# Performance work log

Measured on AMD Instinct MI355X. Metric: run time of the kernel, lower is better.

## Reference

```python
import jax, jax.numpy as jnp
import numpy as np

N_NODES = 10000
N_EDGES = 640000
IN_FEAT = 128
OUT_FEAT = 256


def setup_inputs() -> dict:
    key = jax.random.key(0)
    k_h, k_src, k_dst, k_w, k_b = jax.random.split(key, 5)
    h = jax.random.normal(k_h, (N_NODES, IN_FEAT), dtype=jnp.float32)
    src = jax.random.randint(k_src, (N_EDGES,), 0, N_NODES, dtype=jnp.int64)
    dst = jax.random.randint(k_dst, (N_EDGES,), 0, N_NODES, dtype=jnp.int64)
    W = jax.random.normal(k_w, (2 * IN_FEAT, OUT_FEAT), dtype=jnp.float32) * 0.05
    b = jax.random.normal(k_b, (OUT_FEAT,), dtype=jnp.float32) * 0.05
    return {"h": h, "src": src, "dst": dst, "W": W, "b": b}


def reference(h, src, dst, W, b):
    # Message passing: copy_u('h') then mean-reduce over incoming edges (by dst).
    msgs = h[src]                                   # [E, in_feat] gather
    summed = jax.ops.segment_sum(msgs, dst, num_segments=N_NODES)   # [N, in_feat]
    deg = jax.ops.segment_sum(jnp.ones((src.shape[0],), h.dtype), dst,
                              num_segments=N_NODES)                 # [N]
    h_N = jnp.where(deg[:, None] > 0, summed / jnp.maximum(deg, 1.0)[:, None], 0.0)
    # Concat self + neighbor mean, then dense linear.
    h_total = jnp.concatenate([h, h_N], axis=1)     # [N, 2*in_feat]
    return h_total @ W + b                          # [N, out_feat]
```

## Files before the change

### kernel.cpp

```cpp
#include <hip/hip_runtime.h>
#include <hip/hip_bf16.h>

#define NN 10000
#define NE 640000
#define SB 250
#define EPB 2560
#define NR 625
#define CW 32
#define CE 31
#define CONVB 512
#define ZROW 16000

typedef __attribute__((ext_vector_type(8))) short bf16x8;
typedef __attribute__((ext_vector_type(4))) float f32x4;

__device__ __forceinline__ unsigned packbf(float x, float y) {
  __hip_bfloat16 a = __float2bfloat16(x);
  __hip_bfloat16 c = __float2bfloat16(y);
  unsigned short ua = __builtin_bit_cast(unsigned short, a);
  unsigned short uc = __builtin_bit_cast(unsigned short, c);
  return (unsigned)ua | ((unsigned)uc << 16);
}
__device__ __forceinline__ float blo(unsigned u) { return __uint_as_float(u << 16); }
__device__ __forceinline__ float bhi(unsigned u) { return __uint_as_float(u & 0xffff0000u); }

__global__ __launch_bounds__(256) void kA_scatter_conv(
    const float* __restrict__ h, const int* __restrict__ src,
    const int* __restrict__ dst, const float* __restrict__ W,
    unsigned* __restrict__ gbuf, unsigned* __restrict__ hb32,
    uint4* __restrict__ wpk) {
  int t = threadIdx.x;
  int blk = blockIdx.x;
  if (blk < SB) {
    __shared__ int lc[NR];
    for (int i = t; i < NR; i += 256) lc[i] = 0;
    __syncthreads();
    int base = blk * EPB;
    unsigned dv[10], sv[10];
#pragma unroll
    for (int i = 0; i < 10; i++) {
      int e = base + t + i * 256;
      dv[i] = (unsigned)dst[e] & 0x3fffu;
      sv[i] = (unsigned)src[e] & 0x3fffu;
    }
#pragma unroll
    for (int i = 0; i < 10; i++) {
      int range = (int)(dv[i] >> 4);
      if (range >= NR) range = NR - 1;
      int r = atomicAdd(&lc[range], 1);
      if (r < CE)
        gbuf[((size_t)range * SB + blk) * CW + 1 + r] = ((dv[i] & 15u) << 14) | sv[i];
    }
    __syncthreads();
    for (int i = t; i < NR; i += 256)
      gbuf[((size_t)i * SB + blk) * CW] = (unsigned)lc[i];
  } else {
    int tid = (blk - SB) * 256 + t;
    const float4* h4 = (const float4*)h;
    for (int j = tid; j < NN * 32; j += CONVB * 256) {
      float4 v = h4[j];
      uint2 p;
      p.x = packbf(v.x, v.y);
      p.y = packbf(v.z, v.w);
      *(uint2*)(hb32 + (size_t)j * 2) = p;
    }
    if (tid < 64) hb32[(size_t)ZROW * 64 + tid] = 0u;
    if (tid < 8192) {
      int tt = tid & 255, bnks = tid >> 8;
      int ks = bnks & 7, bn = bnks >> 3;
      int w = tt >> 6, l = tt & 63, kb = l >> 4, lm = l & 15;
      int col = bn * 64 + w * 16 + lm;
      int k0 = ks * 32 + kb * 8;
      uint4 p;
      p.x = packbf(W[(k0 + 0) * 256 + col], W[(k0 + 1) * 256 + col]);
      p.y = packbf(W[(k0 + 2) * 256 + col], W[(k0 + 3) * 256 + col]);
      p.z = packbf(W[(k0 + 4) * 256 + col], W[(k0 + 5) * 256 + col]);
      p.w = packbf(W[(k0 + 6) * 256 + col], W[(k0 + 7) * 256 + col]);
      wpk[tid] = p;
    }
  }
}

__global__ __launch_bounds__(256) void k2_agg_gemm(
    const unsigned* __restrict__ gbuf, const unsigned* __restrict__ hb32,
    const uint4* __restrict__ wpk, const float* __restrict__ bias,
    float* __restrict__ out) {
  __shared__ __align__(16) unsigned short As[16][264];
  __shared__ __align__(16) unsigned short cbuf[16][128];
  __shared__ int lcnt[16];
  __shared__ int tdeg[16];
  int t = threadIdx.x;
  int bm = blockIdx.x;

  const unsigned* chunk = gbuf + ((size_t)bm * SB + (t < SB ? t : SB - 1)) * CW;
  uint4 c0 = *(const uint4*)chunk;
  uint4 c1 = *(const uint4*)(chunk + 4);

  if (t < 16) lcnt[t] = 0;

  {
    int row = t >> 4, c4 = t & 15;
    uint4 v = *(const uint4*)(hb32 + (size_t)(bm * 16 + row) * 64 + c4 * 4);
    *(uint4*)(&As[row][c4 * 8]) = v;
  }
  __syncthreads();

  if (t < SB) {
    int c = (int)(c0.x & 0x3fu);
    int kk = c < CE ? c : CE;
    auto route = [&](unsigned v) {
      int dstlo = (int)(v >> 14) & 15;
      unsigned s = v & 0x3fffu;
      int pos = atomicAdd(&lcnt[dstlo], 1);
      if (pos < 128) cbuf[dstlo][pos] = (unsigned short)s;
    };
    if (kk > 0) route(c0.y);
    if (kk > 1) route(c0.z);
    if (kk > 2) route(c0.w);
    if (kk > 3) route(c1.x);
    if (kk > 4) route(c1.y);
    if (kk > 5) route(c1.z);
    if (kk > 6) route(c1.w);
    for (int j = 7; j < kk; j++) route(chunk[1 + j]);
  }
  __syncthreads();

  if (t < 16) {
    int d = lcnt[t];
    tdeg[t] = d;
    int n = d < 128 ? d : 128;
    int np = (n + 7) & ~7;
    for (int j = n; j < np; j++) cbuf[t][j] = (unsigned short)ZROW;
    lcnt[t] = np;
  }
  __syncthreads();

  int w = t >> 6, l = t & 63;
  int g = l >> 4, lm = l & 15;
#pragma unroll
  for (int i = 0; i < 4; i++) {
    int row = w * 4 + i;
    int np = lcnt[row];
    int deg = tdeg[row];
    float a0 = 0.f, a1 = 0.f, a2 = 0.f, a3 = 0.f;
    float a4 = 0.f, a5 = 0.f, a6 = 0.f, a7 = 0.f;
    for (int e = 0; e < np; e += 8) {
      int s0 = cbuf[row][e + g];
      int s1 = cbuf[row][e + 4 + g];
      uint4 u0 = *(const uint4*)(hb32 + (size_t)s0 * 64 + lm * 4);
      uint4 u1 = *(const uint4*)(hb32 + (size_t)s1 * 64 + lm * 4);
      a0 += blo(u0.x) + blo(u1.x);
      a1 += bhi(u0.x) + bhi(u1.x);
      a2 += blo(u0.y) + blo(u1.y);
      a3 += bhi(u0.y) + bhi(u1.y);
      a4 += blo(u0.z) + blo(u1.z);
      a5 += bhi(u0.z) + bhi(u1.z);
      a6 += blo(u0.w) + blo(u1.w);
      a7 += bhi(u0.w) + bhi(u1.w);
    }
    a0 += __shfl_xor(a0, 16); a1 += __shfl_xor(a1, 16);
    a2 += __shfl_xor(a2, 16); a3 += __shfl_xor(a3, 16);
    a4 += __shfl_xor(a4, 16); a5 += __shfl_xor(a5, 16);
    a6 += __shfl_xor(a6, 16); a7 += __shfl_xor(a7, 16);
    a0 += __shfl_xor(a0, 32); a1 += __shfl_xor(a1, 32);
    a2 += __shfl_xor(a2, 32); a3 += __shfl_xor(a3, 32);
    a4 += __shfl_xor(a4, 32); a5 += __shfl_xor(a5, 32);
    a6 += __shfl_xor(a6, 32); a7 += __shfl_xor(a7, 32);
    float inv = (deg > 0) ? 1.f / (float)deg : 0.f;
    if (g == 0) {
      uint4 p;
      p.x = packbf(a0 * inv, a1 * inv);
      p.y = packbf(a2 * inv, a3 * inv);
      p.z = packbf(a4 * inv, a5 * inv);
      p.w = packbf(a6 * inv, a7 * inv);
      *(uint4*)(&As[row][128 + lm * 8]) = p;
    }
  }
  __syncthreads();

  int kb = g;
#pragma unroll
  for (int bn = 0; bn < 4; bn++) {
    int col = bn * 64 + w * 16 + lm;
    f32x4 acc = (f32x4){0.f, 0.f, 0.f, 0.f};
#pragma unroll
    for (int ks = 0; ks < 8; ks++) {
      uint4 braw = wpk[(bn * 8 + ks) * 256 + t];
      bf16x8 bfr = __builtin_bit_cast(bf16x8, braw);
      uint4 araw = *(const uint4*)(&As[lm][ks * 32 + kb * 8]);
      bf16x8 af = __builtin_bit_cast(bf16x8, araw);
      acc = __builtin_amdgcn_mfma_f32_16x16x32_bf16(af, bfr, acc, 0, 0, 0);
    }
    float biasf = bias[col];
#pragma unroll
    for (int reg = 0; reg < 4; reg++) {
      int m = bm * 16 + kb * 4 + reg;
      out[(size_t)m * 256 + col] = acc[reg] + biasf;
    }
  }
}

extern "C" void kernel_launch(void* const* d_in, const int* in_sizes, int n_in,
                              void* d_out, int out_size, void* d_ws, size_t ws_size,
                              hipStream_t stream) {
  const float* h = (const float*)d_in[0];
  const int* src = (const int*)d_in[1];
  const int* dst = (const int*)d_in[2];
  const float* W = (const float*)d_in[3];
  const float* b = (const float*)d_in[4];
  float* out = (float*)d_out;

  char* ws = (char*)d_ws;
  unsigned* gbuf = (unsigned*)(ws + 0);
  unsigned* hb32 = (unsigned*)(ws + 20000000);
  uint4* wpk = (uint4*)(ws + 24194304);

  kA_scatter_conv<<<SB + CONVB, 256, 0, stream>>>(h, src, dst, W, gbuf, hb32, wpk);
  k2_agg_gemm<<<NR, 256, 0, stream>>>(gbuf, hb32, wpk, b, out);
}
```

Baseline: 96.18 us.

## Halve scatter blocks, prefetch larger edge chunks, unroll gather loop, hoist bias

The edge scatter now uses half as many blocks, each binning twice as many edges. Each (range, block) chunk therefore holds about twice as many entries, and the aggregation kernel has half as many chunks to read. The aggregation kernel prefetches the first 16 words of each chunk into registers, unrolls the neighbour gather to 16 edges per iteration for more loads in flight, and loads the bias before the MFMA loop. The workspace offsets shrink to match the smaller bucket buffer. The risks are more register pressure and a higher chance of a chunk overflowing its 31-entry capacity, although that stays unlikely.

```diff
diff --git a/kernel.cpp b/kernel.cpp
--- a/kernel.cpp
+++ b/kernel.cpp
@@ -3,8 +3,8 @@
 
 #define NN 10000
 #define NE 640000
-#define SB 250
-#define EPB 2560
+#define SB 125
+#define EPB 5120
 #define NR 625
 #define CW 32
 #define CE 31
@@ -36,15 +36,15 @@
     for (int i = t; i < NR; i += 256) lc[i] = 0;
     __syncthreads();
     int base = blk * EPB;
-    unsigned dv[10], sv[10];
-#pragma unroll
-    for (int i = 0; i < 10; i++) {
+    unsigned dv[20], sv[20];
+#pragma unroll
+    for (int i = 0; i < 20; i++) {
       int e = base + t + i * 256;
       dv[i] = (unsigned)dst[e] & 0x3fffu;
       sv[i] = (unsigned)src[e] & 0x3fffu;
     }
 #pragma unroll
-    for (int i = 0; i < 10; i++) {
+    for (int i = 0; i < 20; i++) {
       int range = (int)(dv[i] >> 4);
       if (range >= NR) range = NR - 1;
       int r = atomicAdd(&lc[range], 1);
@@ -91,10 +91,18 @@
   __shared__ int tdeg[16];
   int t = threadIdx.x;
   int bm = blockIdx.x;
+  int w = t >> 6, l = t & 63;
+  int g = l >> 4, lm = l & 15;
 
   const unsigned* chunk = gbuf + ((size_t)bm * SB + (t < SB ? t : SB - 1)) * CW;
   uint4 c0 = *(const uint4*)chunk;
   uint4 c1 = *(const uint4*)(chunk + 4);
+  uint4 c2 = *(const uint4*)(chunk + 8);
+  uint4 c3 = *(const uint4*)(chunk + 12);
+
+  float biasf[4];
+#pragma unroll
+  for (int bn = 0; bn < 4; bn++) biasf[bn] = bias[bn * 64 + w * 16 + lm];
 
   if (t < 16) lcnt[t] = 0;
 
@@ -121,7 +129,15 @@
     if (kk > 4) route(c1.y);
     if (kk > 5) route(c1.z);
     if (kk > 6) route(c1.w);
-    for (int j = 7; j < kk; j++) route(chunk[1 + j]);
+    if (kk > 7) route(c2.x);
+    if (kk > 8) route(c2.y);
+    if (kk > 9) route(c2.z);
+    if (kk > 10) route(c2.w);
+    if (kk > 11) route(c3.x);
+    if (kk > 12) route(c3.y);
+    if (kk > 13) route(c3.z);
+    if (kk > 14) route(c3.w);
+    for (int j = 15; j < kk; j++) route(chunk[1 + j]);
   }
   __syncthreads();
 
@@ -135,8 +151,6 @@
   }
   __syncthreads();
 
-  int w = t >> 6, l = t & 63;
-  int g = l >> 4, lm = l & 15;
 #pragma unroll
   for (int i = 0; i < 4; i++) {
     int row = w * 4 + i;
@@ -144,7 +158,26 @@
     int deg = tdeg[row];
     float a0 = 0.f, a1 = 0.f, a2 = 0.f, a3 = 0.f;
     float a4 = 0.f, a5 = 0.f, a6 = 0.f, a7 = 0.f;
-    for (int e = 0; e < np; e += 8) {
+    int e = 0;
+    for (; e + 15 < np; e += 16) {
+      int s0 = cbuf[row][e + g];
+      int s1 = cbuf[row][e + 4 + g];
+      int s2 = cbuf[row][e + 8 + g];
+      int s3 = cbuf[row][e + 12 + g];
+      uint4 u0 = *(const uint4*)(hb32 + (size_t)s0 * 64 + lm * 4);
+      uint4 u1 = *(const uint4*)(hb32 + (size_t)s1 * 64 + lm * 4);
+      uint4 u2 = *(const uint4*)(hb32 + (size_t)s2 * 64 + lm * 4);
+      uint4 u3 = *(const uint4*)(hb32 + (size_t)s3 * 64 + lm * 4);
+      a0 += (blo(u0.x) + blo(u1.x)) + (blo(u2.x) + blo(u3.x));
+      a1 += (bhi(u0.x) + bhi(u1.x)) + (bhi(u2.x) + bhi(u3.x));
+      a2 += (blo(u0.y) + blo(u1.y)) + (blo(u2.y) + blo(u3.y));
+      a3 += (bhi(u0.y) + bhi(u1.y)) + (bhi(u2.y) + bhi(u3.y));
+      a4 += (blo(u0.z) + blo(u1.z)) + (blo(u2.z) + blo(u3.z));
+      a5 += (bhi(u0.z) + bhi(u1.z)) + (bhi(u2.z) + bhi(u3.z));
+      a6 += (blo(u0.w) + blo(u1.w)) + (blo(u2.w) + blo(u3.w));
+      a7 += (bhi(u0.w) + bhi(u1.w)) + (bhi(u2.w) + bhi(u3.w));
+    }
+    if (e < np) {
       int s0 = cbuf[row][e + g];
       int s1 = cbuf[row][e + 4 + g];
       uint4 u0 = *(const uint4*)(hb32 + (size_t)s0 * 64 + lm * 4);
@@ -191,11 +224,10 @@
       bf16x8 af = __builtin_bit_cast(bf16x8, araw);
       acc = __builtin_amdgcn_mfma_f32_16x16x32_bf16(af, bfr, acc, 0, 0, 0);
     }
-    float biasf = bias[col];
 #pragma unroll
     for (int reg = 0; reg < 4; reg++) {
       int m = bm * 16 + kb * 4 + reg;
-      out[(size_t)m * 256 + col] = acc[reg] + biasf;
+      out[(size_t)m * 256 + col] = acc[reg] + biasf[bn];
     }
   }
 }
@@ -212,8 +244,8 @@
 
   char* ws = (char*)d_ws;
   unsigned* gbuf = (unsigned*)(ws + 0);
-  unsigned* hb32 = (unsigned*)(ws + 20000000);
-  uint4* wpk = (uint4*)(ws + 24194304);
+  unsigned* hb32 = (unsigned*)(ws + 10000000);
+  uint4* wpk = (uint4*)(ws + 14194304);
 
   kA_scatter_conv<<<SB + CONVB, 256, 0, stream>>>(h, src, dst, W, gbuf, hb32, wpk);
   k2_agg_gemm<<<NR, 256, 0, stream>>>(gbuf, hb32, wpk, b, out);
```

Measured after the change: 93.29 us. 3.0% less time.
